# Performance work log

Hardware: AMD Instinct MI355X
Metric: run time of the kernel (lower is better)

Reference implementation:

```python
import jax, jax.numpy as jnp
import numpy as np

EPS = 1e-8  # torch.nn.functional.cosine_similarity default eps


def _l2n(x):
    # normalize along last dim, clamping norm at EPS (matches torch cosine_similarity behavior)
    n = jnp.sqrt(jnp.sum(x * x, axis=-1, keepdims=True))
    return x / jnp.maximum(n, EPS)


def setup_inputs() -> dict:
    key = jax.random.key(0)
    k1, k2 = jax.random.split(key)
    B, n_s, n_q, d = 8, 1024, 2048, 1024
    return {
        "emb_support": jax.random.normal(k1, (B, n_s, d), dtype=jnp.float32),
        "emb_query": jax.random.normal(k2, (B, n_q, d), dtype=jnp.float32),
        "data_support": jnp.zeros((1,), dtype=jnp.float32),
        "data_query": jnp.zeros((1,), dtype=jnp.float32),
    }


def reference(emb_support, emb_query, data_support, data_query):
    # Pairwise cosine similarity via L2-normalize + matmul (avoids O(n^2*d) expand).
    sup_n = _l2n(emb_support)            # [B, n_s, d]
    qry_n = _l2n(emb_query)              # [B, n_q, d]
    cos_support = jnp.einsum('bid,bjd->bij', sup_n, sup_n)  # [B, n_s, n_s]
    cos_query = jnp.einsum('bqd,bjd->bqj', qry_n, sup_n)    # [B, n_q, n_s]
    G_support = jax.nn.softmax(cos_support, axis=-1)
    G_query = jax.nn.softmax(cos_query, axis=-1)
    emb_task_support = jnp.einsum('bij,bjd->bid', G_support, emb_support)
    emb_task_query = jnp.einsum('bqj,bjd->bqd', G_query, emb_support)
    augmented_support = jnp.concatenate([emb_support, emb_task_support], axis=-1)
    augmented_query = jnp.concatenate([emb_query, emb_task_query], axis=-1)
    return (augmented_support, augmented_query, G_support, G_query)
```

## Files before the change

### kernel.cpp

```cpp
#include <hip/hip_runtime.h>
#include <hip/hip_bf16.h>
#include <stdint.h>

#define BATCH 8
#define NS 1024
#define NQ 2048
#define DIM 1024

typedef __bf16 bf16x8 __attribute__((ext_vector_type(8)));
typedef float f32x4 __attribute__((ext_vector_type(4)));

__device__ __forceinline__ unsigned short f2bf(float x) {
    unsigned u = __float_as_uint(x);
    u += 0x7fffu + ((u >> 16) & 1u);
    return (unsigned short)(u >> 16);
}
__device__ __forceinline__ unsigned pk2(float a, float b) {
    return (unsigned)f2bf(a) | ((unsigned)f2bf(b) << 16);
}

#define GL16(gp, lp) __builtin_amdgcn_global_load_lds( \
    (__attribute__((address_space(1))) void*)(gp),     \
    (__attribute__((address_space(3))) void*)(lp), 16, 0, 0)

__global__ __launch_bounds__(256) void normalize_rows(
    const float* __restrict__ in, float* __restrict__ aug,
    unsigned short* __restrict__ nrm)
{
    const int w = threadIdx.x >> 6, lane = threadIdx.x & 63;
    const long long row = (long long)blockIdx.x * 4 + w;
    const float4* in4 = (const float4*)(in + row * DIM);
    float4 v[4];
    float ss = 0.f;
#pragma unroll
    for (int i = 0; i < 4; ++i) {
        v[i] = in4[i * 64 + lane];
        ss += v[i].x * v[i].x + v[i].y * v[i].y + v[i].z * v[i].z + v[i].w * v[i].w;
    }
#pragma unroll
    for (int o = 1; o < 64; o <<= 1) ss += __shfl_xor(ss, o, 64);
    const float scale = 1.0f / fmaxf(sqrtf(ss), 1e-8f);

    float4* aug4 = (float4*)(aug + row * (2 * DIM));
    ushort4* n4 = (ushort4*)(nrm + row * DIM);
#pragma unroll
    for (int i = 0; i < 4; ++i) {
        aug4[i * 64 + lane] = v[i];
        ushort4 u;
        u.x = f2bf(v[i].x * scale);
        u.y = f2bf(v[i].y * scale);
        u.z = f2bf(v[i].z * scale);
        u.w = f2bf(v[i].w * scale);
        n4[i * 64 + lane] = u;
    }
}

__global__ __launch_bounds__(256) void transpose_bf16(
    const float* __restrict__ in, unsigned short* __restrict__ out)
{
    __shared__ unsigned short t[64][65];
    const int b = blockIdx.z;
    const float* src = in + (size_t)b * NS * DIM;
    unsigned short* dst = out + (size_t)b * DIM * NS;
    const int r = threadIdx.x >> 6;
    const int c = threadIdx.x & 63;
    const int rbase = blockIdx.y * 64, cbase = blockIdx.x * 64;
#pragma unroll
    for (int i = 0; i < 16; ++i)
        t[r + i * 4][c] = f2bf(src[(size_t)(rbase + r + i * 4) * DIM + cbase + c]);
    __syncthreads();
#pragma unroll
    for (int i = 0; i < 16; ++i)
        dst[(size_t)(cbase + r + i * 4) * NS + rbase + c] = t[c][r + i * 4];
}

template<bool AF32>
__global__ __launch_bounds__(256) void gemm_abt(
    const void* __restrict__ Ap, const unsigned short* __restrict__ Bp,
    float* __restrict__ Cp,
    long long sA, long long sB, long long sC, int ldc, int coloff)
{
    __shared__ __align__(16) unsigned short As[128 * 32];
    __shared__ __align__(16) unsigned short Bs[128 * 32];
    const int tid = threadIdx.x, lane = tid & 63;
    const int w = tid >> 6, wr = w >> 1, wc = w & 1;
    const int bz = blockIdx.z;
    const unsigned short* B = Bp + (size_t)bz * sB + (size_t)blockIdx.x * 128 * DIM;
    f32x4 acc[4][4] = {};
    const int gr = tid >> 2, gs = (tid & 3) * 8;

    for (int k0 = 0; k0 < DIM; k0 += 32) {
        if (AF32) {
            const float* A = (const float*)Ap + (size_t)bz * sA + (size_t)blockIdx.y * 128 * DIM;
            const int r = tid >> 1, h = (tid & 1) * 16;
            const float4* s4 = (const float4*)(A + (size_t)r * DIM + k0 + h);
            float4 x0 = s4[0], x1 = s4[1], x2 = s4[2], x3 = s4[3];
            uint4 w0 = { pk2(x0.x, x0.y), pk2(x0.z, x0.w), pk2(x1.x, x1.y), pk2(x1.z, x1.w) };
            uint4 w1 = { pk2(x2.x, x2.y), pk2(x2.z, x2.w), pk2(x3.x, x3.y), pk2(x3.z, x3.w) };
            *(uint4*)&As[r * 32 + h] = w0;
            *(uint4*)&As[r * 32 + h + 8] = w1;
        } else {
            const unsigned short* A = (const unsigned short*)Ap + (size_t)bz * sA + (size_t)blockIdx.y * 128 * DIM;
            GL16(A + (size_t)gr * DIM + k0 + gs, As + gr * 32 + gs);
            GL16(A + (size_t)(gr + 64) * DIM + k0 + gs, As + (gr + 64) * 32 + gs);
        }
        GL16(B + (size_t)gr * DIM + k0 + gs, Bs + gr * 32 + gs);
        GL16(B + (size_t)(gr + 64) * DIM + k0 + gs, Bs + (gr + 64) * 32 + gs);
        __syncthreads();

        bf16x8 a[4], b[4];
        const int ks = (lane >> 4) * 8;
#pragma unroll
        for (int m = 0; m < 4; ++m)
            a[m] = *(const bf16x8*)&As[(wr * 64 + m * 16 + (lane & 15)) * 32 + ks];
#pragma unroll
        for (int n = 0; n < 4; ++n)
            b[n] = *(const bf16x8*)&Bs[(wc * 64 + n * 16 + (lane & 15)) * 32 + ks];
#pragma unroll
        for (int m = 0; m < 4; ++m)
#pragma unroll
            for (int n = 0; n < 4; ++n)
                acc[m][n] = __builtin_amdgcn_mfma_f32_16x16x32_bf16(a[m], b[n], acc[m][n], 0, 0, 0);
        __syncthreads();
    }

    float* C = Cp + (size_t)bz * sC;
    const int rb = blockIdx.y * 128 + wr * 64 + ((lane >> 4) << 2);
    const int cb = coloff + blockIdx.x * 128 + wc * 64 + (lane & 15);
#pragma unroll
    for (int m = 0; m < 4; ++m)
#pragma unroll
        for (int n = 0; n < 4; ++n)
#pragma unroll
            for (int j = 0; j < 4; ++j)
                C[(size_t)(rb + m * 16 + j) * ldc + cb + n * 16] = acc[m][n][j];
}

__global__ __launch_bounds__(256) void softmax_rows(float* __restrict__ G)
{
    __shared__ float redm[4], reds[4];
    float4* p = (float4*)(G + (long long)blockIdx.x * 1024);
    const int tid = threadIdx.x, lane = tid & 63, w = tid >> 6;
    float4 v = p[tid];
    float m = fmaxf(fmaxf(v.x, v.y), fmaxf(v.z, v.w));
#pragma unroll
    for (int o = 1; o < 64; o <<= 1) m = fmaxf(m, __shfl_xor(m, o, 64));
    if (lane == 0) redm[w] = m;
    __syncthreads();
    m = fmaxf(fmaxf(redm[0], redm[1]), fmaxf(redm[2], redm[3]));
    float4 e;
    e.x = __expf(v.x - m); e.y = __expf(v.y - m);
    e.z = __expf(v.z - m); e.w = __expf(v.w - m);
    float s = e.x + e.y + e.z + e.w;
#pragma unroll
    for (int o = 1; o < 64; o <<= 1) s += __shfl_xor(s, o, 64);
    if (lane == 0) reds[w] = s;
    __syncthreads();
    s = reds[0] + reds[1] + reds[2] + reds[3];
    const float inv = 1.0f / s;
    e.x *= inv; e.y *= inv; e.z *= inv; e.w *= inv;
    p[tid] = e;
}

extern "C" void kernel_launch(void* const* d_in, const int* in_sizes, int n_in,
                              void* d_out, int out_size, void* d_ws, size_t ws_size,
                              hipStream_t stream)
{
    const float* emb_s = (const float*)d_in[0];
    const float* emb_q = (const float*)d_in[1];
    float* out = (float*)d_out;
    float* aug_s = out;
    float* aug_q = out + (size_t)BATCH * NS * 2 * DIM;
    float* G_s   = aug_q + (size_t)BATCH * NQ * 2 * DIM;
    float* G_q   = G_s + (size_t)BATCH * NS * NS;

    unsigned short* supn = (unsigned short*)d_ws;
    unsigned short* qryn = supn + (size_t)BATCH * NS * DIM;
    unsigned short* embT = qryn + (size_t)BATCH * NQ * DIM;

    normalize_rows<<<BATCH * NS / 4, 256, 0, stream>>>(emb_s, aug_s, supn);
    normalize_rows<<<BATCH * NQ / 4, 256, 0, stream>>>(emb_q, aug_q, qryn);
    transpose_bf16<<<dim3(16, 16, BATCH), 256, 0, stream>>>(emb_s, embT);

    gemm_abt<false><<<dim3(8, 8, BATCH), 256, 0, stream>>>(supn, supn, G_s,
        (long long)NS * DIM, (long long)NS * DIM, (long long)NS * NS, NS, 0);
    gemm_abt<false><<<dim3(8, 16, BATCH), 256, 0, stream>>>(qryn, supn, G_q,
        (long long)NQ * DIM, (long long)NS * DIM, (long long)NQ * NS, NS, 0);

    softmax_rows<<<BATCH * NS, 256, 0, stream>>>(G_s);
    softmax_rows<<<BATCH * NQ, 256, 0, stream>>>(G_q);

    gemm_abt<true><<<dim3(8, 8, BATCH), 256, 0, stream>>>(G_s, embT, aug_s,
        (long long)NS * NS, (long long)DIM * NS, (long long)NS * 2 * DIM, 2 * DIM, DIM);
    gemm_abt<true><<<dim3(8, 16, BATCH), 256, 0, stream>>>(G_q, embT, aug_q,
        (long long)NQ * NS, (long long)DIM * NS, (long long)NQ * 2 * DIM, 2 * DIM, DIM);
}
```

Before: 615.6 us.

## Emit bf16 softmax copy for async LDS loads, swizzle blocks across XCDs, drop max pass

The softmax kernel now also writes a bf16 copy of each probability row into the reused normalized-embedding workspace. The second-stage GEMMs can then use global_load_lds for A instead of loading fp32 and converting to bf16 inside the GEMM, which removes the AF32 template path. The GEMM moves to a 1D grid with an XCD-aware block remap meant to improve L2 locality. Softmax drops its max-reduction pass and subtracts the constant 1, which is safe because cosine similarities are bounded by 1. The cost is an extra bf16 write per softmax row, and the workspace aliasing depends on NS equal to DIM and on kernel ordering.

```diff
diff --git a/kernel.cpp b/kernel.cpp
--- a/kernel.cpp
+++ b/kernel.cpp
@@ -14,9 +14,6 @@
     unsigned u = __float_as_uint(x);
     u += 0x7fffu + ((u >> 16) & 1u);
     return (unsigned short)(u >> 16);
-}
-__device__ __forceinline__ unsigned pk2(float a, float b) {
-    return (unsigned)f2bf(a) | ((unsigned)f2bf(b) << 16);
 }
 
 #define GL16(gp, lp) __builtin_amdgcn_global_load_lds( \
@@ -74,36 +71,32 @@
         dst[(size_t)(cbase + r + i * 4) * NS + rbase + c] = t[c][r + i * 4];
 }
 
-template<bool AF32>
-__global__ __launch_bounds__(256) void gemm_abt(
-    const void* __restrict__ Ap, const unsigned short* __restrict__ Bp,
+__global__ __launch_bounds__(256) void gemm_bt(
+    const unsigned short* __restrict__ Ap, const unsigned short* __restrict__ Bp,
     float* __restrict__ Cp,
-    long long sA, long long sB, long long sC, int ldc, int coloff)
+    long long sA, long long sB, long long sC, int nx, int ny, int ldc, int coloff)
 {
     __shared__ __align__(16) unsigned short As[128 * 32];
     __shared__ __align__(16) unsigned short Bs[128 * 32];
+
+    const int nwg = gridDim.x;
+    const int cpx = nwg >> 3;
+    const int orig = blockIdx.x;
+    const int wg = (orig & 7) * cpx + (orig >> 3);
+    const int per = nx * ny;
+    const int bz = wg / per, rem = wg - bz * per;
+    const int by = rem / nx, bx = rem - by * nx;
+
     const int tid = threadIdx.x, lane = tid & 63;
     const int w = tid >> 6, wr = w >> 1, wc = w & 1;
-    const int bz = blockIdx.z;
-    const unsigned short* B = Bp + (size_t)bz * sB + (size_t)blockIdx.x * 128 * DIM;
+    const unsigned short* A = Ap + (size_t)bz * sA + (size_t)by * 128 * DIM;
+    const unsigned short* B = Bp + (size_t)bz * sB + (size_t)bx * 128 * DIM;
     f32x4 acc[4][4] = {};
     const int gr = tid >> 2, gs = (tid & 3) * 8;
 
     for (int k0 = 0; k0 < DIM; k0 += 32) {
-        if (AF32) {
-            const float* A = (const float*)Ap + (size_t)bz * sA + (size_t)blockIdx.y * 128 * DIM;
-            const int r = tid >> 1, h = (tid & 1) * 16;
-            const float4* s4 = (const float4*)(A + (size_t)r * DIM + k0 + h);
-            float4 x0 = s4[0], x1 = s4[1], x2 = s4[2], x3 = s4[3];
-            uint4 w0 = { pk2(x0.x, x0.y), pk2(x0.z, x0.w), pk2(x1.x, x1.y), pk2(x1.z, x1.w) };
-            uint4 w1 = { pk2(x2.x, x2.y), pk2(x2.z, x2.w), pk2(x3.x, x3.y), pk2(x3.z, x3.w) };
-            *(uint4*)&As[r * 32 + h] = w0;
-            *(uint4*)&As[r * 32 + h + 8] = w1;
-        } else {
-            const unsigned short* A = (const unsigned short*)Ap + (size_t)bz * sA + (size_t)blockIdx.y * 128 * DIM;
-            GL16(A + (size_t)gr * DIM + k0 + gs, As + gr * 32 + gs);
-            GL16(A + (size_t)(gr + 64) * DIM + k0 + gs, As + (gr + 64) * 32 + gs);
-        }
+        GL16(A + (size_t)gr * DIM + k0 + gs, As + gr * 32 + gs);
+        GL16(A + (size_t)(gr + 64) * DIM + k0 + gs, As + (gr + 64) * 32 + gs);
         GL16(B + (size_t)gr * DIM + k0 + gs, Bs + gr * 32 + gs);
         GL16(B + (size_t)(gr + 64) * DIM + k0 + gs, Bs + (gr + 64) * 32 + gs);
         __syncthreads();
@@ -125,8 +118,8 @@
     }
 
     float* C = Cp + (size_t)bz * sC;
-    const int rb = blockIdx.y * 128 + wr * 64 + ((lane >> 4) << 2);
-    const int cb = coloff + blockIdx.x * 128 + wc * 64 + (lane & 15);
+    const int rb = by * 128 + wr * 64 + ((lane >> 4) << 2);
+    const int cb = coloff + bx * 128 + wc * 64 + (lane & 15);
 #pragma unroll
     for (int m = 0; m < 4; ++m)
 #pragma unroll
@@ -136,21 +129,17 @@
                 C[(size_t)(rb + m * 16 + j) * ldc + cb + n * 16] = acc[m][n][j];
 }
 
-__global__ __launch_bounds__(256) void softmax_rows(float* __restrict__ G)
+__global__ __launch_bounds__(256) void softmax_bf(
+    float* __restrict__ G, unsigned short* __restrict__ Gb)
 {
-    __shared__ float redm[4], reds[4];
-    float4* p = (float4*)(G + (long long)blockIdx.x * 1024);
+    __shared__ float reds[4];
+    const long long row = blockIdx.x;
+    float4* p = (float4*)(G + row * 1024);
     const int tid = threadIdx.x, lane = tid & 63, w = tid >> 6;
     float4 v = p[tid];
-    float m = fmaxf(fmaxf(v.x, v.y), fmaxf(v.z, v.w));
-#pragma unroll
-    for (int o = 1; o < 64; o <<= 1) m = fmaxf(m, __shfl_xor(m, o, 64));
-    if (lane == 0) redm[w] = m;
-    __syncthreads();
-    m = fmaxf(fmaxf(redm[0], redm[1]), fmaxf(redm[2], redm[3]));
     float4 e;
-    e.x = __expf(v.x - m); e.y = __expf(v.y - m);
-    e.z = __expf(v.z - m); e.w = __expf(v.w - m);
+    e.x = __expf(v.x - 1.0f); e.y = __expf(v.y - 1.0f);
+    e.z = __expf(v.z - 1.0f); e.w = __expf(v.w - 1.0f);
     float s = e.x + e.y + e.z + e.w;
 #pragma unroll
     for (int o = 1; o < 64; o <<= 1) s += __shfl_xor(s, o, 64);
@@ -160,6 +149,9 @@
     const float inv = 1.0f / s;
     e.x *= inv; e.y *= inv; e.z *= inv; e.w *= inv;
     p[tid] = e;
+    ushort4 u;
+    u.x = f2bf(e.x); u.y = f2bf(e.y); u.z = f2bf(e.z); u.w = f2bf(e.w);
+    ((ushort4*)(Gb + row * 1024))[tid] = u;
 }
 
 extern "C" void kernel_launch(void* const* d_in, const int* in_sizes, int n_in,
@@ -177,21 +169,23 @@
     unsigned short* supn = (unsigned short*)d_ws;
     unsigned short* qryn = supn + (size_t)BATCH * NS * DIM;
     unsigned short* embT = qryn + (size_t)BATCH * NQ * DIM;
+    unsigned short* Gs_bf = supn;
+    unsigned short* Gq_bf = qryn;
 
     normalize_rows<<<BATCH * NS / 4, 256, 0, stream>>>(emb_s, aug_s, supn);
     normalize_rows<<<BATCH * NQ / 4, 256, 0, stream>>>(emb_q, aug_q, qryn);
     transpose_bf16<<<dim3(16, 16, BATCH), 256, 0, stream>>>(emb_s, embT);
 
-    gemm_abt<false><<<dim3(8, 8, BATCH), 256, 0, stream>>>(supn, supn, G_s,
-        (long long)NS * DIM, (long long)NS * DIM, (long long)NS * NS, NS, 0);
-    gemm_abt<false><<<dim3(8, 16, BATCH), 256, 0, stream>>>(qryn, supn, G_q,
-        (long long)NQ * DIM, (long long)NS * DIM, (long long)NQ * NS, NS, 0);
+    gemm_bt<<<8 * 8 * BATCH, 256, 0, stream>>>(supn, supn, G_s,
+        (long long)NS * DIM, (long long)NS * DIM, (long long)NS * NS, 8, 8, NS, 0);
+    gemm_bt<<<8 * 16 * BATCH, 256, 0, stream>>>(qryn, supn, G_q,
+        (long long)NQ * DIM, (long long)NS * DIM, (long long)NQ * NS, 8, 16, NS, 0);
 
-    softmax_rows<<<BATCH * NS, 256, 0, stream>>>(G_s);
-    softmax_rows<<<BATCH * NQ, 256, 0, stream>>>(G_q);
+    softmax_bf<<<BATCH * NS, 256, 0, stream>>>(G_s, Gs_bf);
+    softmax_bf<<<BATCH * NQ, 256, 0, stream>>>(G_q, Gq_bf);
 
-    gemm_abt<true><<<dim3(8, 8, BATCH), 256, 0, stream>>>(G_s, embT, aug_s,
-        (long long)NS * NS, (long long)DIM * NS, (long long)NS * 2 * DIM, 2 * DIM, DIM);
-    gemm_abt<true><<<dim3(8, 16, BATCH), 256, 0, stream>>>(G_q, embT, aug_q,
-        (long long)NQ * NS, (long long)DIM * NS, (long long)NQ * 2 * DIM, 2 * DIM, DIM);
+    gemm_bt<<<8 * 8 * BATCH, 256, 0, stream>>>(Gs_bf, embT, aug_s,
+        (long long)NS * NS, (long long)DIM * NS, (long long)NS * 2 * DIM, 8, 8, 2 * DIM, DIM);
+    gemm_bt<<<8 * 16 * BATCH, 256, 0, stream>>>(Gq_bf, embT, aug_q,
+        (long long)NQ * NS, (long long)DIM * NS, (long long)NQ * 2 * DIM, 8, 16, 2 * DIM, DIM);
 }
```

Measured after the change: 577.9 us. 6.1% less time.
